# Kernel tuning notes

Measured on AMD Instinct MI355X. Metric: run time of the kernel, lower is better.

## Reference

```python
import jax, jax.numpy as jnp
import numpy as np

LN_EPS = 1e-5

def _conv2d(x, w, b, pad):
    # x: [B,C,H,W], w: [O,I,kh,kw] -> [B,O,H,W]
    y = jax.lax.conv_general_dilated(
        x, w, window_strides=(1, 1), padding=[(pad, pad), (pad, pad)],
        dimension_numbers=('NCHW', 'OIHW', 'NCHW'))
    return y + b[None, :, None, None]

def setup_inputs() -> dict:
    key = jax.random.key(0)
    ks = jax.random.split(key, 12)
    B, C, H, W = 4, 256, 64, 64
    D = 64  # inner_projection
    s_in = 1.0 / np.sqrt(C)
    s_d1 = 1.0 / np.sqrt(D)
    s_d3 = 1.0 / np.sqrt(D * 9)
    return {
        'x':     jax.random.normal(ks[0], (B, C, H, W), jnp.float32),
        'w_in':  jax.random.normal(ks[1], (D, C, 1, 1), jnp.float32) * s_in,
        'b_in':  jnp.zeros((D,), jnp.float32),
        'wq':    jax.random.normal(ks[2], (D, D, 3, 3), jnp.float32) * s_d3,
        'bq':    jnp.zeros((D,), jnp.float32),
        'wk':    jax.random.normal(ks[3], (D, D, 3, 3), jnp.float32) * s_d3,
        'bk':    jnp.zeros((D,), jnp.float32),
        'wv':    jax.random.normal(ks[4], (D, D, 3, 3), jnp.float32) * s_d3,
        'bv':    jnp.zeros((D,), jnp.float32),
        'w_out': jax.random.normal(ks[5], (C, D, 1, 1), jnp.float32) * s_d1,
        'b_out': jnp.zeros((C,), jnp.float32),
        'gamma': jax.random.normal(ks[6], (1,), jnp.float32) * 0.1,
        'ln_w':  jnp.ones((C,), jnp.float32),
        'ln_b':  jnp.zeros((C,), jnp.float32),
    }

def _attention(q, k, v):
    # full-pixel attention, NO 1/sqrt(d) scale (matches source)
    B, C, H, W = v.shape
    N = H * W
    qf = q.reshape(B, -1, N)   # [B,d,N]
    kf = k.reshape(B, -1, N)
    vf = v.reshape(B, -1, N)
    energy = jnp.einsum('bci,bcj->bij', qf, kf)      # [B,N,N] = Q^T K
    attn = jax.nn.softmax(energy, axis=-1)
    out = jnp.einsum('bcj,bij->bci', vf, attn)        # V @ attn^T
    return out.reshape(B, C, H, W)

def _layernorm2d(x, w, b):
    # normalize over channel dim per pixel (LayerNorm2d)
    mu = jnp.mean(x, axis=1, keepdims=True)
    var = jnp.var(x, axis=1, keepdims=True)
    xn = (x - mu) * jax.lax.rsqrt(var + LN_EPS)
    return xn * w[None, :, None, None] + b[None, :, None, None]

def reference(x, w_in, b_in, wq, bq, wk, bk, wv, bv, w_out, b_out, gamma, ln_w, ln_b):
    att = _conv2d(x, w_in, b_in, 0)          # inner projection [B,D,H,W]
    q = _conv2d(att, wq, bq, 1)
    k = _conv2d(att, wk, bk, 1)
    v = _conv2d(att, wv, bv, 1)
    att = _attention(q, k, v)
    att = _conv2d(att, w_out, b_out, 0)       # outer projection [B,C,H,W]
    return _layernorm2d(gamma * x + att, ln_w, ln_b)
```

## Files before the change

### kernel.cpp

```cpp
#include <hip/hip_runtime.h>
#include <hip/hip_bf16.h>

#define BB 4
#define CC 256
#define DD 64
#define HH 64
#define WW 64
#define NN 4096
#define NSPLIT 8
#define SM_SHIFT 64.0f

typedef __hip_bfloat16 bf16;
typedef __attribute__((ext_vector_type(8))) short bf16x8;
typedef __attribute__((ext_vector_type(4))) float f32x4;
typedef __attribute__((ext_vector_type(4))) short s16x4;

#define MFMA16(a, b, c) __builtin_amdgcn_mfma_f32_16x16x32_bf16(a, b, c, 0, 0, 0)

static __device__ __forceinline__ float ldin(const void* p, size_t i, bool isb) {
  return isb ? __bfloat162float(((const bf16*)p)[i]) : ((const float*)p)[i];
}
static __device__ __forceinline__ void stout(void* p, size_t i, float v, bool isb) {
  if (isb) ((bf16*)p)[i] = __float2bfloat16(v);
  else     ((float*)p)[i] = v;
}
static __device__ __forceinline__ unsigned pack2(bf16 a, bf16 b) {
  unsigned short ua = *reinterpret_cast<unsigned short*>(&a);
  unsigned short ub = *reinterpret_cast<unsigned short*>(&b);
  return (unsigned)ua | ((unsigned)ub << 16);
}
static __device__ __forceinline__ bool probe_bf16(const unsigned* lnw) {
  return lnw[0] == 0x3F803F80u;
}

__global__ __launch_bounds__(256) void k_wt(
    const void* __restrict__ wq, const void* __restrict__ wk,
    const void* __restrict__ wv, const void* __restrict__ w_in,
    const void* __restrict__ w_out,
    bf16* __restrict__ Wth, bf16* __restrict__ Wtl,
    bf16* __restrict__ Win_h, bf16* __restrict__ Win_l,
    bf16* __restrict__ Wo_h, bf16* __restrict__ Wo_l,
    const unsigned* __restrict__ lnw) {
  const bool isb = probe_bf16(lnw);
  int u = blockIdx.x * 256 + threadIdx.x;
  if (u < 110592) {
    int c3 = u / 36864, rem = u % 36864;
    int tap = rem / 4096, r2 = rem % 4096;
    int oc = r2 >> 6, ic = r2 & 63;
    const void* w = (c3 == 0) ? wq : ((c3 == 1) ? wk : wv);
    float v = ldin(w, (size_t)oc * 576 + ic * 9 + tap, isb);
    bf16 h = __float2bfloat16(v);
    Wth[u] = h;
    Wtl[u] = __float2bfloat16(v - __bfloat162float(h));
  } else if (u < 126976) {
    int v2 = u - 110592;
    float v = ldin(w_in, v2, isb);
    bf16 h = __float2bfloat16(v);
    Win_h[v2] = h;
    Win_l[v2] = __float2bfloat16(v - __bfloat162float(h));
  } else {
    int v2 = u - 126976;
    float v = ldin(w_out, v2, isb);
    bf16 h = __float2bfloat16(v);
    Wo_h[v2] = h;
    Wo_l[v2] = __float2bfloat16(v - __bfloat162float(h));
  }
}

__global__ __launch_bounds__(256) void k_conv_in(
    const void* __restrict__ x,
    const bf16* __restrict__ Win_h, const bf16* __restrict__ Win_l,
    const void* __restrict__ bias, bf16* __restrict__ att_h,
    bf16* __restrict__ att_l, const unsigned* __restrict__ lnw) {
  __shared__ __align__(16) short Xh[32 * 64];
  __shared__ __align__(16) short Xl[32 * 64];
  const bool isb = probe_bf16(lnw);
  const int b = blockIdx.y, n0 = blockIdx.x * 32;
  const int t = threadIdx.x;
  const int w = t >> 6, lane = t & 63, quad = lane >> 4, l16 = lane & 15;
  const int l7 = l16 & 7;
  const size_t xoff = (size_t)b * CC * NN;
  f32x4 acc[2];
  #pragma unroll
  for (int nt = 0; nt < 2; ++nt)
    #pragma unroll
    for (int r = 0; r < 4; ++r)
      acc[nt][r] = ldin(bias, w * 16 + quad * 4 + r, isb);
  for (int c0 = 0; c0 < CC; c0 += 64) {
    __syncthreads();
    #pragma unroll
    for (int i = 0; i < 4; ++i) {
      int u = t + i * 256;
      int dd = u >> 5, n = u & 31;
      float v0 = ldin(x, xoff + (size_t)(c0 + 2 * dd) * NN + n0 + n, isb);
      float v1 = ldin(x, xoff + (size_t)(c0 + 2 * dd + 1) * NN + n0 + n, isb);
      bf16 h0 = __float2bfloat16(v0), h1 = __float2bfloat16(v1);
      bf16 l0 = __float2bfloat16(v0 - __bfloat162float(h0));
      bf16 l1 = __float2bfloat16(v1 - __bfloat162float(h1));
      int cs = ((dd >> 2) ^ (n & 7)) * 8 + ((2 * dd) & 7);
      *(unsigned*)&Xh[n * 64 + cs] = pack2(h0, h1);
      *(unsigned*)&Xl[n * 64 + cs] = pack2(l0, l1);
    }
    __syncthreads();
    #pragma unroll
    for (int kc = 0; kc < 2; ++kc) {
      size_t woff = (size_t)(w * 16 + l16) * 256 + c0 + kc * 32 + quad * 8;
      bf16x8 wh = *(const bf16x8*)(Win_h + woff);
      bf16x8 wl = *(const bf16x8*)(Win_l + woff);
      const int xo = ((kc * 4 + quad) ^ l7) * 8;
      #pragma unroll
      for (int nt = 0; nt < 2; ++nt) {
        int rn = nt * 16 + l16;
        bf16x8 xh = *(const bf16x8*)&Xh[rn * 64 + xo];
        bf16x8 xl = *(const bf16x8*)&Xl[rn * 64 + xo];
        acc[nt] = MFMA16(wh, xh, acc[nt]);
        acc[nt] = MFMA16(wh, xl, acc[nt]);
        acc[nt] = MFMA16(wl, xh, acc[nt]);
      }
    }
  }
  #pragma unroll
  for (int nt = 0; nt < 2; ++nt) {
    size_t off = ((size_t)b * NN + n0 + nt * 16 + l16) * DD + w * 16 + quad * 4;
    bf16 h[4], l[4];
    #pragma unroll
    for (int r = 0; r < 4; ++r) {
      float v = acc[nt][r];
      h[r] = __float2bfloat16(v);
      l[r] = __float2bfloat16(v - __bfloat162float(h[r]));
    }
    *(uint2*)&att_h[off] = make_uint2(pack2(h[0], h[1]), pack2(h[2], h[3]));
    *(uint2*)&att_l[off] = make_uint2(pack2(l[0], l[1]), pack2(l[2], l[3]));
  }
}

__global__ __launch_bounds__(256) void k_conv3(
    const bf16* __restrict__ att_h, const bf16* __restrict__ att_l,
    const bf16* __restrict__ Wth, const bf16* __restrict__ Wtl,
    const void* __restrict__ bq, const void* __restrict__ bk,
    const void* __restrict__ bv,
    bf16* __restrict__ qth, bf16* __restrict__ qtl,
    bf16* __restrict__ kth, bf16* __restrict__ ktl,
    bf16* __restrict__ vt, const unsigned* __restrict__ lnw) {
  __shared__ __align__(16) short Ah[3 * 66 * 64];
  __shared__ __align__(16) short Al[3 * 66 * 64];
  float* o_s = reinterpret_cast<float*>(Ah);
  const bool isb = probe_bf16(lnw);
  const int y = blockIdx.x, b = blockIdx.y, c3 = blockIdx.z;
  const int t = threadIdx.x;
  const int w = t >> 6, lane = t & 63, quad = lane >> 4, l16 = lane & 15;
  const uint4 z4 = make_uint4(0, 0, 0, 0);
  #pragma unroll
  for (int r = 0; r < 3; ++r) {
    int yp = y + r - 1;
    bool ok = (unsigned)yp < 64u;
    const uint4* sh = (const uint4*)(att_h + ((size_t)b * NN + (size_t)yp * 64) * DD);
    const uint4* sl = (const uint4*)(att_l + ((size_t)b * NN + (size_t)yp * 64) * DD);
    #pragma unroll
    for (int ii = 0; ii < 2; ++ii) {
      int u = t + ii * 256;
      int xx = u >> 3, ch = u & 7;
      int rr = r * 66 + xx + 1;
      uint4 vh = ok ? sh[u] : z4;
      uint4 vl = ok ? sl[u] : z4;
      int cs = (ch ^ (rr & 7)) * 8;
      *(uint4*)&Ah[rr * 64 + cs] = vh;
      *(uint4*)&Al[rr * 64 + cs] = vl;
    }
    if (t < 16) {
      int rr = r * 66 + ((t & 1) ? 65 : 0);
      int cs = (t >> 1) * 8;
      *(uint4*)&Ah[rr * 64 + cs] = z4;
      *(uint4*)&Al[rr * 64 + cs] = z4;
    }
  }
  __syncthreads();
  const void* bp = (c3 == 0) ? bq : ((c3 == 1) ? bk : bv);
  const bf16* wth = Wth + (size_t)c3 * 9 * 4096;
  const bf16* wtl = Wtl + (size_t)c3 * 9 * 4096;
  f32x4 acc[4];
  #pragma unroll
  for (int nt = 0; nt < 4; ++nt)
    #pragma unroll
    for (int r = 0; r < 4; ++r)
      acc[nt][r] = ldin(bp, w * 16 + quad * 4 + r, isb);
  #pragma unroll
  for (int tap = 0; tap < 9; ++tap) {
    const int dy = tap / 3, dx = tap % 3;
    const int woff = tap * 4096 + (w * 16 + l16) * 64 + quad * 8;
    bf16x8 wh0 = *(const bf16x8*)(wth + woff);
    bf16x8 wh1 = *(const bf16x8*)(wth + woff + 32);
    bf16x8 wl0 = *(const bf16x8*)(wtl + woff);
    bf16x8 wl1 = *(const bf16x8*)(wtl + woff + 32);
    #pragma unroll
    for (int nt = 0; nt < 4; ++nt) {
      int rr = dy * 66 + nt * 16 + l16 + dx;
      int chA = (quad ^ (rr & 7)) * 8;
      int chB = ((quad + 4) ^ (rr & 7)) * 8;
      bf16x8 ah0 = *(const bf16x8*)&Ah[rr * 64 + chA];
      bf16x8 ah1 = *(const bf16x8*)&Ah[rr * 64 + chB];
      bf16x8 al0 = *(const bf16x8*)&Al[rr * 64 + chA];
      bf16x8 al1 = *(const bf16x8*)&Al[rr * 64 + chB];
      acc[nt] = MFMA16(wh0, ah0, acc[nt]);
      acc[nt] = MFMA16(wh1, ah1, acc[nt]);
      acc[nt] = MFMA16(wh0, al0, acc[nt]);
      acc[nt] = MFMA16(wh1, al1, acc[nt]);
      acc[nt] = MFMA16(wl0, ah0, acc[nt]);
      acc[nt] = MFMA16(wl1, ah1, acc[nt]);
    }
  }
  if (c3 < 2) {
    bf16* dh = (c3 == 0) ? qth : kth;
    bf16* dl = (c3 == 0) ? qtl : ktl;
    const size_t rowb = (size_t)b * NN + (size_t)y * 64;
    #pragma unroll
    for (int nt = 0; nt < 4; ++nt) {
      size_t off = (rowb + nt * 16 + l16) * DD + w * 16 + quad * 4;
      bf16 h[4], l[4];
      #pragma unroll
      for (int r = 0; r < 4; ++r) {
        float v = acc[nt][r];
        h[r] = __float2bfloat16(v);
        l[r] = __float2bfloat16(v - __bfloat162float(h[r]));
      }
      *(uint2*)&dh[off] = make_uint2(pack2(h[0], h[1]), pack2(h[2], h[3]));
      *(uint2*)&dl[off] = make_uint2(pack2(l[0], l[1]), pack2(l[2], l[3]));
    }
  } else {
    __syncthreads();
    #pragma unroll
    for (int nt = 0; nt < 4; ++nt)
      #pragma unroll
      for (int r = 0; r < 4; ++r)
        o_s[(nt * 16 + l16) * 65 + w * 16 + quad * 4 + r] = acc[nt][r];
    __syncthreads();
    #pragma unroll
    for (int i = 0; i < 8; ++i) {
      int u = t + i * 256;
      int c = u >> 5, np = (u & 31) * 2;
      float v0 = o_s[np * 65 + c], v1 = o_s[(np + 1) * 65 + c];
      *(unsigned*)&vt[((size_t)b * DD + c) * NN + (size_t)y * 64 + np] =
          pack2(__float2bfloat16(v0), __float2bfloat16(v1));
    }
  }
}

__global__ __launch_bounds__(256) void k_attn(
    const bf16* __restrict__ qth, const bf16* __restrict__ qtl,
    const bf16* __restrict__ kth, const bf16* __restrict__ ktl,
    const bf16* __restrict__ vt, float* __restrict__ po,
    float* __restrict__ pl) {
  __shared__ __align__(16) short Kh[64 * 64];
  __shared__ __align__(16) short Kl[64 * 64];
  __shared__ __align__(16) short Vs[64 * 64];
  __shared__ __align__(16) short Ps[64 * 64];
  const int b = blockIdx.y, i0 = blockIdx.x * 64, sp = blockIdx.z;
  const int jt0 = sp * (64 / NSPLIT), jt1 = jt0 + (64 / NSPLIT);
  const int t = threadIdx.x;
  const int w = t >> 6, lane = t & 63, quad = lane >> 4, l16 = lane & 15;
  const int l7 = l16 & 7;
  const int xA = (quad ^ l7) * 8;
  const int xB = ((quad + 4) ^ l7) * 8;
  const int sr = t >> 2, m4 = t & 3, sg = m4 * 16;
  const int sc0 = ((2 * m4) ^ (sr & 7)) * 8;
  const int sc1 = ((2 * m4 + 1) ^ (sr & 7)) * 8;
  {
    size_t off = ((size_t)b * NN + i0 + sr) * DD + sg;
    const uint4* qh = (const uint4*)(qth + off);
    const uint4* ql = (const uint4*)(qtl + off);
    *(uint4*)&Kh[sr * 64 + sc0] = qh[0];
    *(uint4*)&Kh[sr * 64 + sc1] = qh[1];
    *(uint4*)&Kl[sr * 64 + sc0] = ql[0];
    *(uint4*)&Kl[sr * 64 + sc1] = ql[1];
  }
  uint4 kh0, kh1, kl0, kl1, vx0, vx1;
  {
    size_t koff = ((size_t)b * NN + jt0 * 64 + sr) * DD + sg;
    kh0 = ((const uint4*)(kth + koff))[0]; kh1 = ((const uint4*)(kth + koff))[1];
    kl0 = ((const uint4*)(ktl + koff))[0]; kl1 = ((const uint4*)(ktl + koff))[1];
    size_t voff = ((size_t)b * DD + sr) * NN + jt0 * 64 + sg;
    vx0 = ((const uint4*)(vt + voff))[0];  vx1 = ((const uint4*)(vt + voff))[1];
  }
  __syncthreads();
  const int rq = w * 16 + l16;
  const bf16x8 qf_h0 = *(const bf16x8*)&Kh[rq * 64 + xA];
  const bf16x8 qf_h1 = *(const bf16x8*)&Kh[rq * 64 + xB];
  const bf16x8 qf_l0 = *(const bf16x8*)&Kl[rq * 64 + xA];
  const bf16x8 qf_l1 = *(const bf16x8*)&Kl[rq * 64 + xB];
  float l_run = 0.f;
  f32x4 oacc[4] = {};
  for (int jt = jt0; jt < jt1; ++jt) {
    __syncthreads();
    *(uint4*)&Kh[sr * 64 + sc0] = kh0;    *(uint4*)&Kh[sr * 64 + sc1] = kh1;
    *(uint4*)&Kl[sr * 64 + sc0] = kl0;    *(uint4*)&Kl[sr * 64 + sc1] = kl1;
    *(uint4*)&Vs[sr * 64 + sc0] = vx0;    *(uint4*)&Vs[sr * 64 + sc1] = vx1;
    __syncthreads();
    if (jt < jt1 - 1) {
      int j0n = (jt + 1) * 64;
      size_t koff = ((size_t)b * NN + j0n + sr) * DD + sg;
      kh0 = ((const uint4*)(kth + koff))[0]; kh1 = ((const uint4*)(kth + koff))[1];
      kl0 = ((const uint4*)(ktl + koff))[0]; kl1 = ((const uint4*)(ktl + koff))[1];
      size_t voff = ((size_t)b * DD + sr) * NN + j0n + sg;
      vx0 = ((const uint4*)(vt + voff))[0];  vx1 = ((const uint4*)(vt + voff))[1];
    }
    f32x4 s[4];
    #pragma unroll
    for (int mt = 0; mt < 4; ++mt) {
      int r0 = (mt * 16 + l16) * 64;
      bf16x8 kf_h0 = *(const bf16x8*)&Kh[r0 + xA];
      bf16x8 kf_h1 = *(const bf16x8*)&Kh[r0 + xB];
      bf16x8 kf_l0 = *(const bf16x8*)&Kl[r0 + xA];
      bf16x8 kf_l1 = *(const bf16x8*)&Kl[r0 + xB];
      f32x4 c = {0.f, 0.f, 0.f, 0.f};
      c = MFMA16(kf_h0, qf_h0, c);
      c = MFMA16(kf_h1, qf_h1, c);
      c = MFMA16(kf_h0, qf_l0, c);
      c = MFMA16(kf_h1, qf_l1, c);
      c = MFMA16(kf_l0, qf_h0, c);
      c = MFMA16(kf_l1, qf_h1, c);
      s[mt] = c;
    }
    float psum = 0.f;
    short pb[16];
    #pragma unroll
    for (int mt = 0; mt < 4; ++mt)
      #pragma unroll
      for (int r = 0; r < 4; ++r) {
        float p = __expf(s[mt][r] - SM_SHIFT);
        bf16 ph = __float2bfloat16(p);
        psum += __bfloat162float(ph);
        pb[mt * 4 + r] = *reinterpret_cast<short*>(&ph);
      }
    psum += __shfl_xor(psum, 16, 64);
    psum += __shfl_xor(psum, 32, 64);
    l_run += psum;
    #pragma unroll
    for (int mt = 0; mt < 4; ++mt) {
      s16x4 pk;
      pk.x = pb[mt * 4 + 0]; pk.y = pb[mt * 4 + 1];
      pk.z = pb[mt * 4 + 2]; pk.w = pb[mt * 4 + 3];
      int chP = ((2 * mt + (quad >> 1)) ^ l7) * 8 + (quad & 1) * 4;
      *(s16x4*)&Ps[rq * 64 + chP] = pk;
    }
    bf16x8 pf0 = *(const bf16x8*)&Ps[rq * 64 + xA];
    bf16x8 pf1 = *(const bf16x8*)&Ps[rq * 64 + xB];
    #pragma unroll
    for (int mt = 0; mt < 4; ++mt) {
      int r0 = (mt * 16 + l16) * 64;
      bf16x8 vf0 = *(const bf16x8*)&Vs[r0 + xA];
      bf16x8 vf1 = *(const bf16x8*)&Vs[r0 + xB];
      oacc[mt] = MFMA16(vf0, pf0, oacc[mt]);
      oacc[mt] = MFMA16(vf1, pf1, oacc[mt]);
    }
  }
  const int ig = i0 + w * 16 + l16;
  const size_t SEGC = (size_t)BB * DD * NN;
  #pragma unroll
  for (int mt = 0; mt < 4; ++mt)
    #pragma unroll
    for (int r = 0; r < 4; ++r) {
      int c = mt * 16 + quad * 4 + r;
      po[(size_t)sp * SEGC + ((size_t)b * DD + c) * NN + ig] = oacc[mt][r];
    }
  if (quad == 0) pl[((size_t)sp * BB + b) * NN + ig] = l_run;
}

__global__ __launch_bounds__(256) void k_out_ln(
    const float* __restrict__ po, const float* __restrict__ pl,
    const void* __restrict__ x,
    const bf16* __restrict__ Wo_h, const bf16* __restrict__ Wo_l,
    const void* __restrict__ bias, const void* __restrict__ gamma,
    const void* __restrict__ lw, const void* __restrict__ lb,
    void* __restrict__ out, const unsigned* __restrict__ lnw) {
  __shared__ __align__(16) short Ahs[32 * 64];
  __shared__ __align__(16) short Als[32 * 64];
  __shared__ float inv_s[32];
  __shared__ float red1[32 * 4], red2[32 * 4];
  __shared__ float mu_s[32], rs_s[32];
  __shared__ float lw_s[256], lb_s[256];
  const bool isb = probe_bf16(lnw);
  const int b = blockIdx.y, n0 = blockIdx.x * 32;
  const int t = threadIdx.x;
  const int w = t >> 6, lane = t & 63, quad = lane >> 4, l16 = lane & 15;
  const int l7 = l16 & 7;
  const size_t SEGC = (size_t)BB * DD * NN;
  if (t < 32) {
    int i = n0 + t;
    float lsum = 0.f;
    #pragma unroll
    for (int s = 0; s < NSPLIT; ++s) lsum += pl[((size_t)s * BB + b) * NN + i];
    inv_s[t] = 1.f / lsum;
  }
  lw_s[t] = ldin(lw, t, isb);
  lb_s[t] = ldin(lb, t, isb);
  const float g = ldin(gamma, 0, isb);
  __syncthreads();
  #pragma unroll
  for (int i = 0; i < 4; ++i) {
    int u = t + i * 256;
    int dd = u >> 5, n = u & 31;
    size_t base = ((size_t)b * DD + 2 * dd) * NN + n0 + n;
    float v0 = 0.f, v1 = 0.f;
    #pragma unroll
    for (int s = 0; s < NSPLIT; ++s) {
      v0 += po[(size_t)s * SEGC + base];
      v1 += po[(size_t)s * SEGC + base + NN];
    }
    float inv = inv_s[n];
    v0 *= inv; v1 *= inv;
    bf16 h0 = __float2bfloat16(v0), h1 = __float2bfloat16(v1);
    bf16 l0 = __float2bfloat16(v0 - __bfloat162float(h0));
    bf16 l1 = __float2bfloat16(v1 - __bfloat162float(h1));
    int cs = ((dd >> 2) ^ (n & 7)) * 8 + ((2 * dd) & 7);
    *(unsigned*)&Ahs[n * 64 + cs] = pack2(h0, h1);
    *(unsigned*)&Als[n * 64 + cs] = pack2(l0, l1);
  }
  f32x4 acc[4][2];
  #pragma unroll
  for (int oct = 0; oct < 4; ++oct)
    #pragma unroll
    for (int r = 0; r < 4; ++r) {
      float bo = ldin(bias, w * 64 + oct * 16 + quad * 4 + r, isb);
      #pragma unroll
      for (int nt = 0; nt < 2; ++nt) acc[oct][nt][r] = bo;
    }
  __syncthreads();
  #pragma unroll
  for (int oct = 0; oct < 4; ++oct) {
    const int base = w * 64 + oct * 16;
    #pragma unroll
    for (int kc = 0; kc < 2; ++kc) {
      size_t woff = (size_t)(base + l16) * 64 + kc * 32 + quad * 8;
      bf16x8 wh = *(const bf16x8*)(Wo_h + woff);
      bf16x8 wl = *(const bf16x8*)(Wo_l + woff);
      const int xo = ((kc * 4 + quad) ^ l7) * 8;
      #pragma unroll
      for (int nt = 0; nt < 2; ++nt) {
        int rn = nt * 16 + l16;
        bf16x8 ah = *(const bf16x8*)&Ahs[rn * 64 + xo];
        bf16x8 al = *(const bf16x8*)&Als[rn * 64 + xo];
        acc[oct][nt] = MFMA16(wh, ah, acc[oct][nt]);
        acc[oct][nt] = MFMA16(wh, al, acc[oct][nt]);
        acc[oct][nt] = MFMA16(wl, ah, acc[oct][nt]);
      }
    }
  }
  #pragma unroll
  for (int nt = 0; nt < 2; ++nt) {
    int nn = nt * 16 + l16;
    float s1 = 0.f, s2 = 0.f;
    #pragma unroll
    for (int oct = 0; oct < 4; ++oct)
      #pragma unroll
      for (int r = 0; r < 4; ++r) {
        int oc = w * 64 + oct * 16 + quad * 4 + r;
        float xv = ldin(x, ((size_t)b * CC + oc) * NN + n0 + nn, isb);
        float y = acc[oct][nt][r] + g * xv;
        acc[oct][nt][r] = y;
        s1 += y; s2 += y * y;
      }
    s1 += __shfl_xor(s1, 16, 64); s1 += __shfl_xor(s1, 32, 64);
    s2 += __shfl_xor(s2, 16, 64); s2 += __shfl_xor(s2, 32, 64);
    if (quad == 0) { red1[nn * 4 + w] = s1; red2[nn * 4 + w] = s2; }
  }
  __syncthreads();
  if (t < 32) {
    float sm = red1[t * 4] + red1[t * 4 + 1] + red1[t * 4 + 2] + red1[t * 4 + 3];
    float sq = red2[t * 4] + red2[t * 4 + 1] + red2[t * 4 + 2] + red2[t * 4 + 3];
    float mu = sm * (1.f / 256.f);
    float var = sq * (1.f / 256.f) - mu * mu;
    mu_s[t] = mu;
    rs_s[t] = rsqrtf(var + 1e-5f);
  }
  __syncthreads();
  #pragma unroll
  for (int nt = 0; nt < 2; ++nt) {
    int nn = nt * 16 + l16;
    float mu = mu_s[nn], rs = rs_s[nn];
    #pragma unroll
    for (int oct = 0; oct < 4; ++oct)
      #pragma unroll
      for (int r = 0; r < 4; ++r) {
        int oc = w * 64 + oct * 16 + quad * 4 + r;
        float o = (acc[oct][nt][r] - mu) * rs * lw_s[oc] + lb_s[oc];
        stout(out, ((size_t)b * CC + oc) * NN + n0 + nn, o, isb);
      }
  }
}

extern "C" void kernel_launch(void* const* d_in, const int* in_sizes, int n_in,
                              void* d_out, int out_size, void* d_ws, size_t ws_size,
                              hipStream_t stream) {
  const void* x     = d_in[0];
  const void* w_in  = d_in[1];
  const void* b_in  = d_in[2];
  const void* wq    = d_in[3];
  const void* bq    = d_in[4];
  const void* wk    = d_in[5];
  const void* bk    = d_in[6];
  const void* wv    = d_in[7];
  const void* bv    = d_in[8];
  const void* w_out = d_in[9];
  const void* b_out = d_in[10];
  const void* gamma = d_in[11];
  const void* ln_w  = d_in[12];
  const void* ln_b  = d_in[13];

  const size_t SEG = (size_t)BB * DD * NN;
  char*  p     = (char*)d_ws;
  bf16*  att_h = (bf16*)p;  p += SEG * 2;
  bf16*  att_l = (bf16*)p;  p += SEG * 2;
  bf16*  qth   = (bf16*)p;  p += SEG * 2;
  bf16*  qtl   = (bf16*)p;  p += SEG * 2;
  bf16*  kth   = (bf16*)p;  p += SEG * 2;
  bf16*  ktl   = (bf16*)p;  p += SEG * 2;
  bf16*  vt    = (bf16*)p;  p += SEG * 2;
  float* po    = (float*)p; p += (size_t)NSPLIT * SEG * 4;
  float* pl    = (float*)p; p += (size_t)NSPLIT * BB * NN * 4;
  bf16*  Wth   = (bf16*)p;  p += 110592 * 2;
  bf16*  Wtl   = (bf16*)p;  p += 110592 * 2;
  bf16*  Win_h = (bf16*)p;  p += 16384 * 2;
  bf16*  Win_l = (bf16*)p;  p += 16384 * 2;
  bf16*  Wo_h  = (bf16*)p;  p += 16384 * 2;
  bf16*  Wo_l  = (bf16*)p;  p += 16384 * 2;
  const unsigned* lnw = (const unsigned*)ln_w;

  k_wt<<<560, 256, 0, stream>>>(wq, wk, wv, w_in, w_out, Wth, Wtl,
                                Win_h, Win_l, Wo_h, Wo_l, lnw);
  k_conv_in<<<dim3(NN / 32, BB), 256, 0, stream>>>(x, Win_h, Win_l, b_in,
                                                   att_h, att_l, lnw);
  k_conv3<<<dim3(64, BB, 3), 256, 0, stream>>>(att_h, att_l, Wth, Wtl,
                                               bq, bk, bv,
                                               qth, qtl, kth, ktl, vt, lnw);
  k_attn<<<dim3(NN / 64, BB, NSPLIT), 256, 0, stream>>>(qth, qtl, kth, ktl, vt,
                                                        po, pl);
  k_out_ln<<<dim3(NN / 32, BB), 256, 0, stream>>>(po, pl, x, Wo_h, Wo_l,
                                                  b_out, gamma, ln_w, ln_b,
                                                  d_out, lnw);
}
```

Before: 186.3 us.

## Process 128 query rows per attention block, keep P in registers, use exp2

The attention kernel now handles two 64-row query subtiles per block, so each K/V tile staged in shared memory is reused twice and the grid shrinks by half. The probability tile no longer round-trips through shared memory: the score accumulator layout is fed straight into 16x16x16 bf16 MFMAs as the B operand. Q is prescaled by log2(e) in the conv kernel so the softmax can use a native exp2 with an equivalently adjusted shift. This raises register pressure (twice the accumulators and Q fragments) and halves block count, which may reduce occupancy.

```diff
diff --git a/kernel.cpp b/kernel.cpp
--- a/kernel.cpp
+++ b/kernel.cpp
@@ -8,7 +8,8 @@
 #define WW 64
 #define NN 4096
 #define NSPLIT 8
-#define SM_SHIFT 64.0f
+#define SM_SHIFT2 92.332482616893664f
+#define LOG2E 1.4426950408889634f
 
 typedef __hip_bfloat16 bf16;
 typedef __attribute__((ext_vector_type(8))) short bf16x8;
@@ -16,6 +17,25 @@
 typedef __attribute__((ext_vector_type(4))) short s16x4;
 
 #define MFMA16(a, b, c) __builtin_amdgcn_mfma_f32_16x16x32_bf16(a, b, c, 0, 0, 0)
+
+#if __has_builtin(__builtin_amdgcn_mfma_f32_16x16x16bf16_1k)
+static __device__ __forceinline__ f32x4 MFMA16K(s16x4 a, s16x4 b, f32x4 c) {
+  return __builtin_amdgcn_mfma_f32_16x16x16bf16_1k(a, b, c, 0, 0, 0);
+}
+#else
+static __device__ __forceinline__ f32x4 MFMA16K(s16x4 a, s16x4 b, f32x4 c) {
+  f32x4 d;
+  asm("v_mfma_f32_16x16x16_bf16 %0, %1, %2, %3"
+      : "=&v"(d) : "v"(a), "v"(b), "v"(c));
+  return d;
+}
+#endif
+
+#if __has_builtin(__builtin_amdgcn_exp2f)
+#define EXP2F(x) __builtin_amdgcn_exp2f(x)
+#else
+#define EXP2F(x) exp2f(x)
+#endif
 
 static __device__ __forceinline__ float ldin(const void* p, size_t i, bool isb) {
   return isb ? __bfloat162float(((const bf16*)p)[i]) : ((const float*)p)[i];
@@ -212,6 +232,7 @@
   if (c3 < 2) {
     bf16* dh = (c3 == 0) ? qth : kth;
     bf16* dl = (c3 == 0) ? qtl : ktl;
+    const float qsc = (c3 == 0) ? LOG2E : 1.0f;
     const size_t rowb = (size_t)b * NN + (size_t)y * 64;
     #pragma unroll
     for (int nt = 0; nt < 4; ++nt) {
@@ -219,7 +240,7 @@
       bf16 h[4], l[4];
       #pragma unroll
       for (int r = 0; r < 4; ++r) {
-        float v = acc[nt][r];
+        float v = acc[nt][r] * qsc;
         h[r] = __float2bfloat16(v);
         l[r] = __float2bfloat16(v - __bfloat162float(h[r]));
       }
@@ -253,8 +274,7 @@
   __shared__ __align__(16) short Kh[64 * 64];
   __shared__ __align__(16) short Kl[64 * 64];
   __shared__ __align__(16) short Vs[64 * 64];
-  __shared__ __align__(16) short Ps[64 * 64];
-  const int b = blockIdx.y, i0 = blockIdx.x * 64, sp = blockIdx.z;
+  const int b = blockIdx.y, i0 = blockIdx.x * 128, sp = blockIdx.z;
   const int jt0 = sp * (64 / NSPLIT), jt1 = jt0 + (64 / NSPLIT);
   const int t = threadIdx.x;
   const int w = t >> 6, lane = t & 63, quad = lane >> 4, l16 = lane & 15;
@@ -264,14 +284,14 @@
   const int sr = t >> 2, m4 = t & 3, sg = m4 * 16;
   const int sc0 = ((2 * m4) ^ (sr & 7)) * 8;
   const int sc1 = ((2 * m4 + 1) ^ (sr & 7)) * 8;
-  {
-    size_t off = ((size_t)b * NN + i0 + sr) * DD + sg;
-    const uint4* qh = (const uint4*)(qth + off);
-    const uint4* ql = (const uint4*)(qtl + off);
-    *(uint4*)&Kh[sr * 64 + sc0] = qh[0];
-    *(uint4*)&Kh[sr * 64 + sc1] = qh[1];
-    *(uint4*)&Kl[sr * 64 + sc0] = ql[0];
-    *(uint4*)&Kl[sr * 64 + sc1] = ql[1];
+  bf16x8 qf_h0[2], qf_h1[2], qf_l0[2], qf_l1[2];
+  #pragma unroll
+  for (int is = 0; is < 2; ++is) {
+    size_t qoff = ((size_t)b * NN + i0 + is * 64 + w * 16 + l16) * DD + quad * 8;
+    qf_h0[is] = *(const bf16x8*)(qth + qoff);
+    qf_h1[is] = *(const bf16x8*)(qth + qoff + 32);
+    qf_l0[is] = *(const bf16x8*)(qtl + qoff);
+    qf_l1[is] = *(const bf16x8*)(qtl + qoff + 32);
   }
   uint4 kh0, kh1, kl0, kl1, vx0, vx1;
   {
@@ -281,14 +301,8 @@
     size_t voff = ((size_t)b * DD + sr) * NN + jt0 * 64 + sg;
     vx0 = ((const uint4*)(vt + voff))[0];  vx1 = ((const uint4*)(vt + voff))[1];
   }
-  __syncthreads();
-  const int rq = w * 16 + l16;
-  const bf16x8 qf_h0 = *(const bf16x8*)&Kh[rq * 64 + xA];
-  const bf16x8 qf_h1 = *(const bf16x8*)&Kh[rq * 64 + xB];
-  const bf16x8 qf_l0 = *(const bf16x8*)&Kl[rq * 64 + xA];
-  const bf16x8 qf_l1 = *(const bf16x8*)&Kl[rq * 64 + xB];
-  float l_run = 0.f;
-  f32x4 oacc[4] = {};
+  float l_run[2] = {0.f, 0.f};
+  f32x4 oacc[4][2] = {};
   for (int jt = jt0; jt < jt1; ++jt) {
     __syncthreads();
     *(uint4*)&Kh[sr * 64 + sc0] = kh0;    *(uint4*)&Kh[sr * 64 + sc1] = kh1;
@@ -303,7 +317,8 @@
       size_t voff = ((size_t)b * DD + sr) * NN + j0n + sg;
       vx0 = ((const uint4*)(vt + voff))[0];  vx1 = ((const uint4*)(vt + voff))[1];
     }
-    f32x4 s[4];
+    s16x4 pf[2][4];
+    float psum[2] = {0.f, 0.f};
     #pragma unroll
     for (int mt = 0; mt < 4; ++mt) {
       int r0 = (mt * 16 + l16) * 64;
@@ -311,58 +326,60 @@
       bf16x8 kf_h1 = *(const bf16x8*)&Kh[r0 + xB];
       bf16x8 kf_l0 = *(const bf16x8*)&Kl[r0 + xA];
       bf16x8 kf_l1 = *(const bf16x8*)&Kl[r0 + xB];
-      f32x4 c = {0.f, 0.f, 0.f, 0.f};
-      c = MFMA16(kf_h0, qf_h0, c);
-      c = MFMA16(kf_h1, qf_h1, c);
-      c = MFMA16(kf_h0, qf_l0, c);
-      c = MFMA16(kf_h1, qf_l1, c);
-      c = MFMA16(kf_l0, qf_h0, c);
-      c = MFMA16(kf_l1, qf_h1, c);
-      s[mt] = c;
-    }
-    float psum = 0.f;
-    short pb[16];
+      #pragma unroll
+      for (int is = 0; is < 2; ++is) {
+        f32x4 c = {0.f, 0.f, 0.f, 0.f};
+        c = MFMA16(kf_h0, qf_h0[is], c);
+        c = MFMA16(kf_h1, qf_h1[is], c);
+        c = MFMA16(kf_h0, qf_l0[is], c);
+        c = MFMA16(kf_h1, qf_l1[is], c);
+        c = MFMA16(kf_l0, qf_h0[is], c);
+        c = MFMA16(kf_l1, qf_h1[is], c);
+        s16x4 pk;
+        float ps = 0.f;
+        #pragma unroll
+        for (int r = 0; r < 4; ++r) {
+          float p = EXP2F(c[r] - SM_SHIFT2);
+          bf16 ph = __float2bfloat16(p);
+          ps += __bfloat162float(ph);
+          pk[r] = *reinterpret_cast<short*>(&ph);
+        }
+        psum[is] += ps;
+        pf[is][mt] = pk;
+      }
+    }
+    #pragma unroll
+    for (int is = 0; is < 2; ++is) {
+      float ps = psum[is];
+      ps += __shfl_xor(ps, 16, 64);
+      ps += __shfl_xor(ps, 32, 64);
+      l_run[is] += ps;
+    }
+    #pragma unroll
+    for (int mt = 0; mt < 4; ++mt) {
+      int rv = (mt * 16 + l16) * 64;
+      #pragma unroll
+      for (int kt = 0; kt < 4; ++kt) {
+        s16x4 vf = *(const s16x4*)
+            &Vs[rv + ((kt * 2 + (quad >> 1)) ^ l7) * 8 + (quad & 1) * 4];
+        oacc[mt][0] = MFMA16K(vf, pf[0][kt], oacc[mt][0]);
+        oacc[mt][1] = MFMA16K(vf, pf[1][kt], oacc[mt][1]);
+      }
+    }
+  }
+  const size_t SEGC = (size_t)BB * DD * NN;
+  #pragma unroll
+  for (int is = 0; is < 2; ++is) {
+    const int ig = i0 + is * 64 + w * 16 + l16;
     #pragma unroll
     for (int mt = 0; mt < 4; ++mt)
       #pragma unroll
       for (int r = 0; r < 4; ++r) {
-        float p = __expf(s[mt][r] - SM_SHIFT);
-        bf16 ph = __float2bfloat16(p);
-        psum += __bfloat162float(ph);
-        pb[mt * 4 + r] = *reinterpret_cast<short*>(&ph);
-      }
-    psum += __shfl_xor(psum, 16, 64);
-    psum += __shfl_xor(psum, 32, 64);
-    l_run += psum;
-    #pragma unroll
-    for (int mt = 0; mt < 4; ++mt) {
-      s16x4 pk;
-      pk.x = pb[mt * 4 + 0]; pk.y = pb[mt * 4 + 1];
-      pk.z = pb[mt * 4 + 2]; pk.w = pb[mt * 4 + 3];
-      int chP = ((2 * mt + (quad >> 1)) ^ l7) * 8 + (quad & 1) * 4;
-      *(s16x4*)&Ps[rq * 64 + chP] = pk;
-    }
-    bf16x8 pf0 = *(const bf16x8*)&Ps[rq * 64 + xA];
-    bf16x8 pf1 = *(const bf16x8*)&Ps[rq * 64 + xB];
-    #pragma unroll
-    for (int mt = 0; mt < 4; ++mt) {
-      int r0 = (mt * 16 + l16) * 64;
-      bf16x8 vf0 = *(const bf16x8*)&Vs[r0 + xA];
-      bf16x8 vf1 = *(const bf16x8*)&Vs[r0 + xB];
-      oacc[mt] = MFMA16(vf0, pf0, oacc[mt]);
-      oacc[mt] = MFMA16(vf1, pf1, oacc[mt]);
-    }
-  }
-  const int ig = i0 + w * 16 + l16;
-  const size_t SEGC = (size_t)BB * DD * NN;
-  #pragma unroll
-  for (int mt = 0; mt < 4; ++mt)
-    #pragma unroll
-    for (int r = 0; r < 4; ++r) {
-      int c = mt * 16 + quad * 4 + r;
-      po[(size_t)sp * SEGC + ((size_t)b * DD + c) * NN + ig] = oacc[mt][r];
-    }
-  if (quad == 0) pl[((size_t)sp * BB + b) * NN + ig] = l_run;
+        int c = mt * 16 + quad * 4 + r;
+        po[(size_t)sp * SEGC + ((size_t)b * DD + c) * NN + ig] = oacc[mt][is][r];
+      }
+    if (quad == 0) pl[((size_t)sp * BB + b) * NN + ig] = l_run[is];
+  }
 }
 
 __global__ __launch_bounds__(256) void k_out_ln(
@@ -532,8 +549,8 @@
   k_conv3<<<dim3(64, BB, 3), 256, 0, stream>>>(att_h, att_l, Wth, Wtl,
                                                bq, bk, bv,
                                                qth, qtl, kth, ktl, vt, lnw);
-  k_attn<<<dim3(NN / 64, BB, NSPLIT), 256, 0, stream>>>(qth, qtl, kth, ktl, vt,
-                                                        po, pl);
+  k_attn<<<dim3(NN / 128, BB, NSPLIT), 256, 0, stream>>>(qth, qtl, kth, ktl, vt,
+                                                         po, pl);
   k_out_ln<<<dim3(NN / 32, BB), 256, 0, stream>>>(po, pl, x, Wo_h, Wo_l,
                                                   b_out, gamma, ln_w, ln_b,
                                                   d_out, lnw);
```

New measurement: 177.2 us. 4.9% less time.
